# Performance work log

Measured on AMD Instinct MI355X. Metric: run time of the kernel, lower is better.

Reference implementation:

```python
import jax, jax.numpy as jnp
import numpy as np
from jax import lax

B = 2
H = W = 128          # resolution
N = H * W            # 16384 tokens
C = 128              # in_channels
C2 = C // 2          # 64, attention dim
G = 16               # window_size
HEADS = 8
HDIM = C2 // HEADS   # 8
EPS = 1e-5
DN = ('NCHW', 'OIHW', 'NCHW')


def setup_inputs():
    key = jax.random.key(0)
    ks = jax.random.split(key, 16)
    r = lambda i, shape, s=0.02: jax.random.normal(ks[i], shape, jnp.float32) * s
    z = lambda shape: jnp.zeros(shape, jnp.float32)
    o = lambda shape: jnp.ones(shape, jnp.float32)
    return {
        'x_C': jax.random.normal(ks[0], (B, N, C), jnp.float32),
        'x_T': jax.random.normal(ks[1], (B, N, C), jnp.float32),
        # S_conv = depthwise 3x3 + pointwise 1x1
        'conv1_dw': r(2, (C, 1, 3, 3)), 'conv1_dw_b': z((C,)),
        'conv1_pw': r(3, (C, C, 1, 1)), 'conv1_pw_b': z((C,)),
        'bn1_gamma': o((C,)), 'bn1_beta': z((C,)),
        'bn1_mean': r(4, (C,), 0.1), 'bn1_var': jnp.abs(r(5, (C,), 0.1)) + 1.0,
        'enc_W': r(6, (C, C2)), 'enc_b': z((C2,)),
        'pos': r(7, (1, N, C2)),
        'ln_gamma': o((C2,)), 'ln_beta': z((C2,)),
        'qkv_W': r(8, (C2, 3 * C2)),                      # qkv_bias=False
        'proj_W': r(9, (C2, C2)), 'proj_b': z((C2,)),
        'ffn_W1': r(10, (C2, C2)), 'ffn_b1': z((C2,)),
        'ffn_W2': r(11, (C2, C2)), 'ffn_b2': z((C2,)),
        'dec_W': r(12, (C2, C)), 'dec_b': z((C,)),
    }


def _ln(x, g, b):
    m = jnp.mean(x, -1, keepdims=True)
    v = jnp.var(x, -1, keepdims=True)
    return (x - m) * jax.lax.rsqrt(v + EPS) * g + b


def _win_part(x):  # (B,N,C2) -> (B*nW, G*G, C2)
    x = x.reshape(B, H // G, G, W // G, G, C2).transpose(0, 1, 3, 2, 4, 5)
    return x.reshape(-1, G * G, C2)


def _win_rev(x):  # (B*nW, G*G, C2) -> (B,N,C2)
    x = x.reshape(B, H // G, W // G, G, G, C2).transpose(0, 1, 3, 2, 4, 5)
    return x.reshape(B, N, C2)


def reference(x_C, x_T, conv1_dw, conv1_dw_b, conv1_pw, conv1_pw_b,
              bn1_gamma, bn1_beta, bn1_mean, bn1_var,
              enc_W, enc_b, pos, ln_gamma, ln_beta, qkv_W,
              proj_W, proj_b, ffn_W1, ffn_b1, ffn_W2, ffn_b2, dec_W, dec_b):
    cb = lambda a: a[None, :, None, None]
    # ---- CNN branch on x_C: S_conv -> BN(eval) -> ReLU, residual
    xC = x_C.reshape(B, H, W, C).transpose(0, 3, 1, 2)  # NCHW
    h = lax.conv_general_dilated(xC, conv1_dw, (1, 1), 'SAME',
                                 feature_group_count=C, dimension_numbers=DN) + cb(conv1_dw_b)
    h = lax.conv_general_dilated(h, conv1_pw, (1, 1), 'SAME',
                                 dimension_numbers=DN) + cb(conv1_pw_b)
    h = (h - cb(bn1_mean)) * cb(bn1_gamma * jax.lax.rsqrt(bn1_var + EPS)) + cb(bn1_beta)
    x1 = jax.nn.relu(h) + xC
    # ---- x_T branch: source overwrites conv/bn outputs -> x2 = relu(x_T) + x_T
    xT = x_T.reshape(B, H, W, C).transpose(0, 3, 1, 2)
    x2 = jax.nn.relu(xT) + xT
    # ---- flatten to tokens, encode + positional embedding
    x = x1.transpose(0, 2, 3, 1).reshape(B, N, C)
    y = x2.transpose(0, 2, 3, 1).reshape(B, N, C)
    x_poi = x @ enc_W + enc_b + pos
    y_poi = y @ enc_W + enc_b + pos
    # ---- window partition + LayerNorm
    wx = _ln(_win_part(x_poi), ln_gamma, ln_beta)
    wy = _ln(_win_part(y_poi), ln_gamma, ln_beta)
    # ---- dual-stream windowed attention (cross values)
    scale = HDIM ** -0.5
    def qkv(t):
        q, k, v = jnp.split(t @ qkv_W, 3, axis=-1)
        re = lambda a: a.reshape(-1, G * G, HEADS, HDIM).transpose(0, 2, 1, 3)
        return re(q), re(k), re(v)
    q, k, v = qkv(wx)
    q1, k1, v1 = qkv(wy)
    attn = jax.nn.softmax(jnp.einsum('bhid,bhjd->bhij', q * scale, k), axis=-1)
    attn1 = jax.nn.softmax(jnp.einsum('bhid,bhjd->bhij', q1 * scale, k1), axis=-1)
    ox = jnp.einsum('bhij,bhjd->bhid', attn, v1).transpose(0, 2, 1, 3).reshape(-1, G * G, C2)
    oy = jnp.einsum('bhij,bhjd->bhid', attn1, v).transpose(0, 2, 1, 3).reshape(-1, G * G, C2)
    ox = ox @ proj_W + proj_b + wx
    oy = oy @ proj_W + proj_b + wy
    # ---- window reverse + FFN (pre-LN, residual)
    x = _win_rev(ox)
    y = _win_rev(oy)
    ffn = lambda t: jax.nn.relu(_ln(t, ln_gamma, ln_beta) @ ffn_W1 + ffn_b1) @ ffn_W2 + ffn_b2
    x = x + ffn(x)
    y = y + ffn(y)
    # ---- decode back to C channels; to_3d(reshape) is identity on (B,N,C)
    return (x @ dec_W + dec_b) + (y @ dec_W + dec_b)
```

## Files before the change

### kernel.cpp

```cpp
#include <hip/hip_runtime.h>
#include <hip/hip_bf16.h>
#include <math.h>

#define EPSF 1e-5f
#define KSCL 0.51010090329771713f

#if __has_builtin(__builtin_amdgcn_exp2f)
#define EXP2(x) __builtin_amdgcn_exp2f(x)
#else
#define EXP2(x) exp2f(x)
#endif

typedef __attribute__((ext_vector_type(8))) short short8;
typedef __attribute__((ext_vector_type(16))) float f32x16;

__device__ __forceinline__ unsigned int f2bf(float f) {
    union { float f; unsigned int i; } u; u.f = f;
    unsigned int r = u.i + 0x7FFFu + ((u.i >> 16) & 1u);
    return r >> 16;
}
__device__ __forceinline__ unsigned cvtpk(float a, float b) {
    unsigned r;
    asm("v_cvt_pk_bf16_f32 %0, %1, %2" : "=v"(r) : "v"(a), "v"(b));
    return r;
}
__device__ __forceinline__ void bbuild(const unsigned pk[8], int lh,
                                       short8& B0, short8& B1) {
    unsigned xs[8];
    #pragma unroll
    for (int i = 0; i < 8; ++i) xs[i] = (unsigned)__shfl_xor((int)pk[i], 32);
    uint4 w0, w1;
    w0.x = lh ? xs[2] : pk[0]; w0.y = lh ? xs[3] : pk[1];
    w0.z = lh ? pk[2] : xs[0]; w0.w = lh ? pk[3] : xs[1];
    w1.x = lh ? xs[6] : pk[4]; w1.y = lh ? xs[7] : pk[5];
    w1.z = lh ? pk[6] : xs[4]; w1.w = lh ? pk[7] : xs[5];
    B0 = __builtin_bit_cast(short8, w0);
    B1 = __builtin_bit_cast(short8, w1);
}

__global__ __launch_bounds__(256) void k_dwconv(
    const float* __restrict__ xC, const float* __restrict__ dwW,
    const float* __restrict__ dwB, unsigned short* __restrict__ xdwb,
    const float* __restrict__ qkvW, const float* __restrict__ pw,
    const float* __restrict__ pwb, const float* __restrict__ gam,
    const float* __restrict__ bet, const float* __restrict__ mean,
    const float* __restrict__ var, const float* __restrict__ projW,
    const float* __restrict__ W1, const float* __restrict__ W2,
    const float* __restrict__ decW,
    unsigned short* __restrict__ qkvWT, unsigned short* __restrict__ weff,
    float* __restrict__ beff, unsigned short* __restrict__ projWTn,
    unsigned short* __restrict__ W1Tn, unsigned short* __restrict__ W2Tn,
    unsigned short* __restrict__ decTn)
{
    int tid = threadIdx.x;
    int bid = blockIdx.x;
    if (bid >= 1024) {
        int pid = (bid - 1024) * 256 + tid;
        if (pid < 12288) {
            int o = pid >> 6, c = pid & 63;
            qkvWT[pid] = (unsigned short)f2bf(qkvW[c * 192 + o]);
        } else if (pid < 28672) {
            int i = pid - 12288;
            int co = i >> 7;
            float sc = gam[co] * rsqrtf(var[co] + EPSF);
            weff[i] = (unsigned short)f2bf(pw[i] * sc);
        } else if (pid < 32768) {
            int i = pid - 28672, m = i >> 6, c = i & 63;
            projWTn[i] = (unsigned short)f2bf(projW[c * 64 + m]);
        } else if (pid < 36864) {
            int i = pid - 32768, m = i >> 6, c = i & 63;
            W1Tn[i] = (unsigned short)f2bf(W1[c * 64 + m]);
        } else if (pid < 40960) {
            int i = pid - 36864, m = i >> 6, c = i & 63;
            W2Tn[i] = (unsigned short)f2bf(W2[c * 64 + m]);
        } else if (pid < 49152) {
            int i = pid - 40960, m = i >> 6, c = i & 63;
            decTn[i] = (unsigned short)f2bf(decW[c * 128 + m]);
        } else if (pid < 49280) {
            int i = pid - 49152;
            float sc = gam[i] * rsqrtf(var[i] + EPSF);
            beff[i] = (pwb[i] - mean[i]) * sc + bet[i];
        }
        return;
    }
    __shared__ float s_w[128 * 9];
    __shared__ float s_bias[128];
    for (int i = tid; i < 128 * 9; i += 256) s_w[i] = dwW[i];
    if (tid < 128) s_bias[tid] = dwB[tid];
    __syncthreads();
    int idx = bid * 256 + tid;
    int c4 = (idx & 31) * 4;
    int pg = idx >> 5;
    int t0 = pg * 4;
    int b = t0 >> 14, n = t0 & 16383;
    int row = n >> 7, col0 = n & 127;
    float vb[3][6][4];
    #pragma unroll
    for (int ky = 0; ky < 3; ++ky) {
        int r = row + ky - 1;
        #pragma unroll
        for (int cx = 0; cx < 6; ++cx) {
            int cl = col0 + cx - 1;
            if ((unsigned)r < 128u && (unsigned)cl < 128u) {
                *(float4*)&vb[ky][cx][0] =
                    *(const float4*)&xC[((size_t)(b << 14) + (r << 7) + cl) * 128 + c4];
            } else {
                vb[ky][cx][0] = 0.f; vb[ky][cx][1] = 0.f; vb[ky][cx][2] = 0.f; vb[ky][cx][3] = 0.f;
            }
        }
    }
    float acc[4][4];
    #pragma unroll
    for (int p = 0; p < 4; ++p)
        #pragma unroll
        for (int j = 0; j < 4; ++j) acc[p][j] = s_bias[c4 + j];
    #pragma unroll
    for (int ky = 0; ky < 3; ++ky)
        #pragma unroll
        for (int kx = 0; kx < 3; ++kx)
            #pragma unroll
            for (int j = 0; j < 4; ++j) {
                float w = s_w[(c4 + j) * 9 + ky * 3 + kx];
                #pragma unroll
                for (int p = 0; p < 4; ++p)
                    acc[p][j] = fmaf(w, vb[ky][p + kx][j], acc[p][j]);
            }
    #pragma unroll
    for (int p = 0; p < 4; ++p) {
        uint2 o;
        o.x = f2bf(acc[p][0]) | (f2bf(acc[p][1]) << 16);
        o.y = f2bf(acc[p][2]) | (f2bf(acc[p][3]) << 16);
        *(uint2*)&xdwb[((size_t)t0 + p) * 128 + c4] = o;
    }
}

__global__ __launch_bounds__(256) void k_pw(
    const unsigned short* __restrict__ xdwb, const float* __restrict__ xC,
    const unsigned short* __restrict__ weff, const float* __restrict__ beff,
    float* __restrict__ x1)
{
    int tid = threadIdx.x;
    int wv = tid >> 6, lane = tid & 63, l31 = lane & 31, lh = lane >> 5;
    int wr = wv >> 1, wc = wv & 1;
    int T0 = blockIdx.x * 64;
    int ta = T0 + wr * 32 + l31;
    short8 af[8];
    #pragma unroll
    for (int ks = 0; ks < 8; ++ks)
        af[ks] = *(const short8*)&xdwb[(size_t)ta * 128 + ks * 16 + lh * 8];
    #pragma unroll
    for (int nt = 0; nt < 2; ++nt) {
        int co = wc * 64 + nt * 32 + l31;
        f32x16 acc = {};
        #pragma unroll
        for (int ks = 0; ks < 8; ++ks) {
            short8 bfr = *(const short8*)&weff[(size_t)co * 128 + ks * 16 + lh * 8];
            acc = __builtin_amdgcn_mfma_f32_32x32x16_bf16(af[ks], bfr, acc, 0, 0, 0);
        }
        float be = beff[co];
        #pragma unroll
        for (int r = 0; r < 16; ++r) {
            int tt = T0 + wr * 32 + (r & 3) + 8 * (r >> 2) + 4 * lh;
            float v = fmaxf(acc[r] + be, 0.f) + xC[(size_t)tt * 128 + co];
            x1[(size_t)tt * 128 + co] = v;
        }
    }
}

__global__ __launch_bounds__(512) void k_encln(
    const float* __restrict__ x1, const float* __restrict__ xT,
    const float* __restrict__ encW, const float* __restrict__ encb,
    const float* __restrict__ pos, const float* __restrict__ lng,
    const float* __restrict__ lnb, float* __restrict__ wx, float* __restrict__ wy,
    unsigned short* __restrict__ wxb, unsigned short* __restrict__ wyb)
{
    __shared__ float s_in[64 * 128];
    __shared__ float s_w[128 * 64];
    int tid = threadIdx.x;
    int T0 = blockIdx.x * 64;
    int stream = blockIdx.y;
    for (int i = tid; i < 2048; i += 512) ((float4*)s_w)[i] = ((const float4*)encW)[i];
    if (stream == 0) {
        for (int i = tid; i < 2048; i += 512)
            ((float4*)s_in)[i] = ((const float4*)(x1 + (size_t)T0 * 128))[i];
    } else {
        for (int i = tid; i < 2048; i += 512) {
            float4 v = ((const float4*)(xT + (size_t)T0 * 128))[i];
            float4 o;
            o.x = v.x > 0.f ? 2.f * v.x : v.x;
            o.y = v.y > 0.f ? 2.f * v.y : v.y;
            o.z = v.z > 0.f ? 2.f * v.z : v.z;
            o.w = v.w > 0.f ? 2.f * v.w : v.w;
            ((float4*)s_in)[i] = o;
        }
    }
    __syncthreads();
    int q = tid & 15, o4 = q * 4;
    int tg = tid >> 4;
    float acc[2][4] = {};
    for (int ci = 0; ci < 128; ++ci) {
        float4 w = *(const float4*)&s_w[ci * 64 + o4];
        #pragma unroll
        for (int i = 0; i < 2; ++i) {
            float xin = s_in[(tg * 2 + i) * 128 + ci];
            acc[i][0] = fmaf(xin, w.x, acc[i][0]);
            acc[i][1] = fmaf(xin, w.y, acc[i][1]);
            acc[i][2] = fmaf(xin, w.z, acc[i][2]);
            acc[i][3] = fmaf(xin, w.w, acc[i][3]);
        }
    }
    float4 eb = *(const float4*)&encb[o4];
    float4 g  = *(const float4*)&lng[o4];
    float4 bb = *(const float4*)&lnb[o4];
    float* dst = stream == 0 ? wx : wy;
    unsigned short* dstb = stream == 0 ? wxb : wyb;
    #pragma unroll
    for (int i = 0; i < 2; ++i) {
        int t = T0 + tg * 2 + i;
        int n = t & 16383;
        float4 pv = *(const float4*)&pos[(size_t)n * 64 + o4];
        float v0 = acc[i][0] + eb.x + pv.x;
        float v1 = acc[i][1] + eb.y + pv.y;
        float v2 = acc[i][2] + eb.z + pv.z;
        float v3 = acc[i][3] + eb.w + pv.w;
        float sm = v0 + v1 + v2 + v3;
        float sq = v0 * v0 + v1 * v1 + v2 * v2 + v3 * v3;
        #pragma unroll
        for (int off = 1; off < 16; off <<= 1) {
            sm += __shfl_xor(sm, off);
            sq += __shfl_xor(sq, off);
        }
        float m = sm * (1.f / 64.f);
        float vr = sq * (1.f / 64.f) - m * m;
        float rs = rsqrtf(fmaxf(vr, 0.f) + EPSF);
        float4 o;
        o.x = (v0 - m) * rs * g.x + bb.x;
        o.y = (v1 - m) * rs * g.y + bb.y;
        o.z = (v2 - m) * rs * g.z + bb.z;
        o.w = (v3 - m) * rs * g.w + bb.w;
        *(float4*)&dst[(size_t)t * 64 + o4] = o;
        uint2 ob;
        ob.x = f2bf(o.x) | (f2bf(o.y) << 16);
        ob.y = f2bf(o.z) | (f2bf(o.w) << 16);
        *(uint2*)&dstb[(size_t)t * 64 + o4] = ob;
    }
}

__global__ __launch_bounds__(256) void k_qkv(
    const unsigned short* __restrict__ wxb, const unsigned short* __restrict__ wyb,
    const unsigned short* __restrict__ qkvWT,
    unsigned short* __restrict__ qk, unsigned short* __restrict__ vT)
{
    int tid = threadIdx.x;
    int wv = tid >> 6, lane = tid & 63, l31 = lane & 31, lh = lane >> 5;
    int s = blockIdx.y;
    int T0 = blockIdx.x * 128;
    int b = T0 >> 14;
    int row = (T0 & 16383) >> 7;
    const unsigned short* src = s ? wyb : wxb;
    int t = T0 + wv * 32 + l31;
    short8 bfr[4];
    #pragma unroll
    for (int ks = 0; ks < 4; ++ks)
        bfr[ks] = *(const short8*)&src[(size_t)t * 64 + ks * 16 + lh * 8];
    int cp = wv * 32 + l31;
    int wid = ((row >> 4) << 3) + (cp >> 4);
    int p = ((row & 15) << 4) + (cp & 15);
    size_t cb = (size_t)(s * 2 + b) * 512 + wid;
    #pragma unroll
    for (int nt = 0; nt < 6; ++nt) {
        f32x16 acc = {};
        #pragma unroll
        for (int ks = 0; ks < 4; ++ks) {
            short8 afr = *(const short8*)&qkvWT[(size_t)(nt * 32 + l31) * 64 + ks * 16 + lh * 8];
            acc = __builtin_amdgcn_mfma_f32_32x32x16_bf16(afr, bfr[ks], acc, 0, 0, 0);
        }
        if (nt < 4) {
            const float scl = nt < 2 ? 1.f : KSCL;
            const int sec = nt < 2 ? 0 : 1;
            #pragma unroll
            for (int g = 0; g < 4; ++g) {
                int head = (nt & 1) * 4 + g;
                unsigned short* rec = qk + (cb + head * 64) * 4096;
                float f0 = acc[4 * g + 0] * scl, f1 = acc[4 * g + 1] * scl;
                float f2 = acc[4 * g + 2] * scl, f3 = acc[4 * g + 3] * scl;
                unsigned u01 = cvtpk(f0, f1), u23 = cvtpk(f2, f3);
                int off = p * 16 + sec * 8 + 4 * lh;
                *(unsigned*)(rec + off) = u01;
                *(unsigned*)(rec + off + 2) = u23;
            }
        } else {
            #pragma unroll
            for (int g = 0; g < 4; ++g) {
                int head = (nt - 4) * 4 + g;
                unsigned short* vrec = vT + (cb + head * 64) * 2048;
                int d0 = 4 * lh;
                vrec[(d0 + 0) * 256 + p] = (unsigned short)f2bf(acc[4 * g + 0]);
                vrec[(d0 + 1) * 256 + p] = (unsigned short)f2bf(acc[4 * g + 1]);
                vrec[(d0 + 2) * 256 + p] = (unsigned short)f2bf(acc[4 * g + 2]);
                vrec[(d0 + 3) * 256 + p] = (unsigned short)f2bf(acc[4 * g + 3]);
            }
        }
    }
}

__global__ __launch_bounds__(256) void k_attn(
    const unsigned short* __restrict__ qk, const unsigned short* __restrict__ vT,
    float* __restrict__ ox, float* __restrict__ oy)
{
    int tid = threadIdx.x;
    int wave = tid >> 6, lane = tid & 63;
    int lh = lane >> 5, l31 = lane & 31;
    int bx = blockIdx.x;
    int s = bx >> 10;
    int r = bx & 1023;
    int head = (r >> 6) & 7, wid = r & 63, b = r >> 9;
    const unsigned short* qbase = qk + ((size_t)s * 1024 + r) * 4096;
    const unsigned short* vbase = vT + ((size_t)(s ^ 1) * 1024 + r) * 2048;

    short8 qf[2];
    #pragma unroll
    for (int qt = 0; qt < 2; ++qt) {
        uint4 v = {0u, 0u, 0u, 0u};
        if (lh == 0) v = *(const uint4*)(qbase + (size_t)(wave * 64 + qt * 32 + l31) * 16);
        qf[qt] = __builtin_bit_cast(short8, v);
    }
    f32x16 acc[2];
    #pragma unroll
    for (int qt = 0; qt < 2; ++qt) acc[qt] = (f32x16){};
    const unsigned ONES = 0x3F803F80u;

    for (int jt = 0; jt < 8; ++jt) {
        uint4 kv = {0u, 0u, 0u, 0u};
        if (lh == 0) kv = *(const uint4*)(qbase + (size_t)(jt * 32 + l31) * 16 + 8);
        short8 kf = __builtin_bit_cast(short8, kv);
        uint2 a0 = {ONES, ONES}, a1 = {ONES, ONES}, a2 = {ONES, ONES}, a3 = {ONES, ONES};
        if (l31 < 8) {
            const unsigned short* vp = vbase + l31 * 256 + jt * 32 + lh * 4;
            a0 = *(const uint2*)vp;
            a1 = *(const uint2*)(vp + 8);
            a2 = *(const uint2*)(vp + 16);
            a3 = *(const uint2*)(vp + 24);
        }
        uint4 vaw = {a0.x, a0.y, a1.x, a1.y};
        uint4 vbw = {a2.x, a2.y, a3.x, a3.y};
        short8 vf0 = __builtin_bit_cast(short8, vaw);
        short8 vf1 = __builtin_bit_cast(short8, vbw);
        #pragma unroll
        for (int qt = 0; qt < 2; ++qt) {
            f32x16 c = __builtin_amdgcn_mfma_f32_32x32x16_bf16(kf, qf[qt], (f32x16){}, 0, 0, 0);
            float p[16];
            #pragma unroll
            for (int i = 0; i < 16; ++i) p[i] = EXP2(c[i]);
            unsigned pk[8];
            #pragma unroll
            for (int i = 0; i < 8; ++i) pk[i] = cvtpk(p[2 * i], p[2 * i + 1]);
            uint4 bw0 = {pk[0], pk[1], pk[2], pk[3]};
            uint4 bw1 = {pk[4], pk[5], pk[6], pk[7]};
            short8 B0 = __builtin_bit_cast(short8, bw0);
            short8 B1 = __builtin_bit_cast(short8, bw1);
            acc[qt] = __builtin_amdgcn_mfma_f32_32x32x16_bf16(vf0, B0, acc[qt], 0, 0, 0);
            acc[qt] = __builtin_amdgcn_mfma_f32_32x32x16_bf16(vf1, B1, acc[qt], 0, 0, 0);
        }
    }
    float* dst = s ? oy : ox;
    #pragma unroll
    for (int qt = 0; qt < 2; ++qt) {
        float inv = 1.f / acc[qt][4];
        int p = wave * 64 + qt * 32 + l31;
        int orow = (wid >> 3) * 16 + (p >> 4);
        int ocol = (wid & 7) * 16 + (p & 15);
        size_t t = (size_t)b * 16384 + orow * 128 + ocol;
        float4 o;
        o.x = acc[qt][0] * inv; o.y = acc[qt][1] * inv;
        o.z = acc[qt][2] * inv; o.w = acc[qt][3] * inv;
        *(float4*)&dst[t * 64 + head * 8 + lh * 4] = o;
    }
}

__global__ __launch_bounds__(256) void k_fusedec(
    const float* __restrict__ ox, const float* __restrict__ oy,
    const float* __restrict__ wx, const float* __restrict__ wy,
    const unsigned short* __restrict__ projWTn, const float* __restrict__ projb,
    const unsigned short* __restrict__ W1Tn, const float* __restrict__ b1,
    const unsigned short* __restrict__ W2Tn, const float* __restrict__ b2,
    const unsigned short* __restrict__ decTn, const float* __restrict__ decb,
    const float* __restrict__ lng, const float* __restrict__ lnb,
    float* __restrict__ out)
{
    int tid = threadIdx.x;
    int wv = tid >> 6, l31 = tid & 31, lh = (tid >> 5) & 1;
    int t = blockIdx.x * 128 + wv * 32 + l31;
    f32x16 zacc[2];
    zacc[0] = (f32x16){}; zacc[1] = (f32x16){};
    #pragma unroll 1
    for (int s = 0; s < 2; ++s) {
        const float* osrc = s ? oy : ox;
        const float* wsrc = s ? wy : wx;
        short8 bo[4];
        #pragma unroll
        for (int kap = 0; kap < 4; ++kap) {
            float4 f0 = *(const float4*)&osrc[(size_t)t * 64 + kap * 16 + lh * 8];
            float4 f1 = *(const float4*)&osrc[(size_t)t * 64 + kap * 16 + lh * 8 + 4];
            uint4 w;
            w.x = cvtpk(f0.x, f0.y); w.y = cvtpk(f0.z, f0.w);
            w.z = cvtpk(f1.x, f1.y); w.w = cvtpk(f1.z, f1.w);
            bo[kap] = __builtin_bit_cast(short8, w);
        }
        f32x16 a1[2];
        #pragma unroll
        for (int ta = 0; ta < 2; ++ta) {
            f32x16 acc = {};
            #pragma unroll
            for (int kap = 0; kap < 4; ++kap) {
                short8 af = *(const short8*)&projWTn[(size_t)(ta * 32 + l31) * 64 + kap * 16 + lh * 8];
                acc = __builtin_amdgcn_mfma_f32_32x32x16_bf16(af, bo[kap], acc, 0, 0, 0);
            }
            #pragma unroll
            for (int g = 0; g < 4; ++g) {
                int c0 = ta * 32 + g * 8 + lh * 4;
                float4 pb = *(const float4*)&projb[c0];
                float4 wr = *(const float4*)&wsrc[(size_t)t * 64 + c0];
                acc[g * 4 + 0] += pb.x + wr.x;
                acc[g * 4 + 1] += pb.y + wr.y;
                acc[g * 4 + 2] += pb.z + wr.z;
                acc[g * 4 + 3] += pb.w + wr.w;
            }
            a1[ta] = acc;
        }
        float sm = 0.f, sq = 0.f;
        #pragma unroll
        for (int ta = 0; ta < 2; ++ta)
            #pragma unroll
            for (int r = 0; r < 16; ++r) { float v = a1[ta][r]; sm += v; sq += v * v; }
        sm += __shfl_xor(sm, 32); sq += __shfl_xor(sq, 32);
        float mu = sm * (1.f / 64.f);
        float rs = rsqrtf(fmaxf(sq * (1.f / 64.f) - mu * mu, 0.f) + EPSF);
        unsigned pku[2][8];
        #pragma unroll
        for (int ta = 0; ta < 2; ++ta)
            #pragma unroll
            for (int g = 0; g < 4; ++g) {
                int c0 = ta * 32 + g * 8 + lh * 4;
                float4 gg = *(const float4*)&lng[c0];
                float4 bb = *(const float4*)&lnb[c0];
                float u0 = (a1[ta][g * 4 + 0] - mu) * rs * gg.x + bb.x;
                float u1 = (a1[ta][g * 4 + 1] - mu) * rs * gg.y + bb.y;
                float u2 = (a1[ta][g * 4 + 2] - mu) * rs * gg.z + bb.z;
                float u3 = (a1[ta][g * 4 + 3] - mu) * rs * gg.w + bb.w;
                pku[ta][g * 2]     = cvtpk(u0, u1);
                pku[ta][g * 2 + 1] = cvtpk(u2, u3);
            }
        short8 Bu[4];
        bbuild(pku[0], lh, Bu[0], Bu[1]);
        bbuild(pku[1], lh, Bu[2], Bu[3]);
        unsigned pkh[2][8];
        #pragma unroll
        for (int th = 0; th < 2; ++th) {
            f32x16 acc = {};
            #pragma unroll
            for (int kap = 0; kap < 4; ++kap) {
                short8 af = *(const short8*)&W1Tn[(size_t)(th * 32 + l31) * 64 + kap * 16 + lh * 8];
                acc = __builtin_amdgcn_mfma_f32_32x32x16_bf16(af, Bu[kap], acc, 0, 0, 0);
            }
            #pragma unroll
            for (int g = 0; g < 4; ++g) {
                int c0 = th * 32 + g * 8 + lh * 4;
                float4 bb = *(const float4*)&b1[c0];
                float h0 = fmaxf(acc[g * 4 + 0] + bb.x, 0.f);
                float h1 = fmaxf(acc[g * 4 + 1] + bb.y, 0.f);
                float h2 = fmaxf(acc[g * 4 + 2] + bb.z, 0.f);
                float h3 = fmaxf(acc[g * 4 + 3] + bb.w, 0.f);
                pkh[th][g * 2]     = cvtpk(h0, h1);
                pkh[th][g * 2 + 1] = cvtpk(h2, h3);
            }
        }
        short8 Bh[4];
        bbuild(pkh[0], lh, Bh[0], Bh[1]);
        bbuild(pkh[1], lh, Bh[2], Bh[3]);
        #pragma unroll
        for (int ta = 0; ta < 2; ++ta) {
            f32x16 a3 = a1[ta];
            #pragma unroll
            for (int g = 0; g < 4; ++g) {
                int c0 = ta * 32 + g * 8 + lh * 4;
                float4 bb = *(const float4*)&b2[c0];
                a3[g * 4 + 0] += bb.x; a3[g * 4 + 1] += bb.y;
                a3[g * 4 + 2] += bb.z; a3[g * 4 + 3] += bb.w;
            }
            #pragma unroll
            for (int kap = 0; kap < 4; ++kap) {
                short8 af = *(const short8*)&W2Tn[(size_t)(ta * 32 + l31) * 64 + kap * 16 + lh * 8];
                a3 = __builtin_amdgcn_mfma_f32_32x32x16_bf16(af, Bh[kap], a3, 0, 0, 0);
            }
            zacc[ta] += a3;
        }
    }
    unsigned pkz[2][8];
    #pragma unroll
    for (int ta = 0; ta < 2; ++ta)
        #pragma unroll
        for (int g = 0; g < 4; ++g) {
            pkz[ta][g * 2]     = cvtpk(zacc[ta][g * 4 + 0], zacc[ta][g * 4 + 1]);
            pkz[ta][g * 2 + 1] = cvtpk(zacc[ta][g * 4 + 2], zacc[ta][g * 4 + 3]);
        }
    short8 Bz[4];
    bbuild(pkz[0], lh, Bz[0], Bz[1]);
    bbuild(pkz[1], lh, Bz[2], Bz[3]);
    #pragma unroll
    for (int mu4 = 0; mu4 < 4; ++mu4) {
        f32x16 a4 = {};
        #pragma unroll
        for (int g = 0; g < 4; ++g) {
            int c0 = mu4 * 32 + g * 8 + lh * 4;
            float4 db = *(const float4*)&decb[c0];
            a4[g * 4 + 0] = 2.f * db.x; a4[g * 4 + 1] = 2.f * db.y;
            a4[g * 4 + 2] = 2.f * db.z; a4[g * 4 + 3] = 2.f * db.w;
        }
        #pragma unroll
        for (int kap = 0; kap < 4; ++kap) {
            short8 af = *(const short8*)&decTn[(size_t)(mu4 * 32 + l31) * 64 + kap * 16 + lh * 8];
            a4 = __builtin_amdgcn_mfma_f32_32x32x16_bf16(af, Bz[kap], a4, 0, 0, 0);
        }
        #pragma unroll
        for (int g = 0; g < 4; ++g) {
            int c0 = mu4 * 32 + g * 8 + lh * 4;
            float4 o;
            o.x = a4[g * 4 + 0]; o.y = a4[g * 4 + 1];
            o.z = a4[g * 4 + 2]; o.w = a4[g * 4 + 3];
            *(float4*)&out[(size_t)t * 128 + c0] = o;
        }
    }
}

extern "C" void kernel_launch(void* const* d_in, const int* in_sizes, int n_in,
                              void* d_out, int out_size, void* d_ws, size_t ws_size,
                              hipStream_t stream) {
    const float* x_C   = (const float*)d_in[0];
    const float* x_T   = (const float*)d_in[1];
    const float* dwW   = (const float*)d_in[2];
    const float* dwB   = (const float*)d_in[3];
    const float* pw    = (const float*)d_in[4];
    const float* pwb   = (const float*)d_in[5];
    const float* gam   = (const float*)d_in[6];
    const float* bet   = (const float*)d_in[7];
    const float* mean  = (const float*)d_in[8];
    const float* var   = (const float*)d_in[9];
    const float* encW  = (const float*)d_in[10];
    const float* encb  = (const float*)d_in[11];
    const float* pos   = (const float*)d_in[12];
    const float* lng   = (const float*)d_in[13];
    const float* lnb   = (const float*)d_in[14];
    const float* qkvW  = (const float*)d_in[15];
    const float* projW = (const float*)d_in[16];
    const float* projb = (const float*)d_in[17];
    const float* W1    = (const float*)d_in[18];
    const float* b1    = (const float*)d_in[19];
    const float* W2    = (const float*)d_in[20];
    const float* b2    = (const float*)d_in[21];
    const float* decW  = (const float*)d_in[22];
    const float* decb  = (const float*)d_in[23];
    float* out = (float*)d_out;

    float* ws = (float*)d_ws;
    unsigned short* xdwb = (unsigned short*)ws;
    float* x1   = ws + 2097152;
    unsigned short* qkb  = (unsigned short*)(ws + 6291456);
    unsigned short* vTb  = (unsigned short*)(ws + 10485760);
    float* wx   = ws + 12582912;
    float* wy   = ws + 14680064;
    unsigned short* wxb = (unsigned short*)(ws + 16777216);
    unsigned short* wyb = (unsigned short*)(ws + 17825792);
    float* ox   = ws + 18874368;
    float* oy   = ws + 20971520;
    unsigned short* qkvWT   = (unsigned short*)(ws + 23068672);
    unsigned short* weff    = (unsigned short*)(ws + 23074816);
    float*          beff    = ws + 23083008;
    unsigned short* projWTn = (unsigned short*)(ws + 23083136);
    unsigned short* W1Tn    = (unsigned short*)(ws + 23085184);
    unsigned short* W2Tn    = (unsigned short*)(ws + 23087232);
    unsigned short* decTn   = (unsigned short*)(ws + 23089280);

    k_dwconv<<<1217, 256, 0, stream>>>(x_C, dwW, dwB, xdwb, qkvW, pw, pwb,
                                       gam, bet, mean, var, projW, W1, W2, decW,
                                       qkvWT, weff, beff, projWTn, W1Tn, W2Tn, decTn);
    k_pw<<<512, 256, 0, stream>>>(xdwb, x_C, weff, beff, x1);
    k_encln<<<dim3(512, 2), 512, 0, stream>>>(x1, x_T, encW, encb, pos, lng, lnb,
                                              wx, wy, wxb, wyb);
    k_qkv<<<dim3(256, 2), 256, 0, stream>>>(wxb, wyb, qkvWT, qkb, vTb);
    k_attn<<<2048, 256, 0, stream>>>(qkb, vTb, ox, oy);
    k_fusedec<<<256, 256, 0, stream>>>(ox, oy, wx, wy, projWTn, projb,
                                       W1Tn, b1, W2Tn, b2, decTn, decb,
                                       lng, lnb, out);
}
```

Before: 113.6 us.

## Move encoder projection to bf16 MFMA and drop fp32 intermediates

The encoder linear plus LayerNorm kernel, previously a scalar FP32 shared-memory GEMM, now runs on bf16 MFMA 32x32x16 with the encoder weight pre-transposed to bf16 in the prep kernel. The pointwise-conv output x1 is now stored as bf16 instead of fp32. The fp32 copies of wx/wy are no longer written, and the fused decode kernel reads the residual from the bf16 buffers. This cuts memory traffic and ALU time in the encoder stage, at the cost of extra bf16 rounding on x1 and on the attention residual.

Result: faster. 100.8 us (-11.3%).

```diff
diff --git a/kernel.cpp b/kernel.cpp
--- a/kernel.cpp
+++ b/kernel.cpp
@@ -14,6 +14,9 @@
 typedef __attribute__((ext_vector_type(8))) short short8;
 typedef __attribute__((ext_vector_type(16))) float f32x16;
 
+__device__ __forceinline__ float bf2f(unsigned short u) {
+    union { unsigned int i; float f; } x; x.i = ((unsigned int)u) << 16; return x.f;
+}
 __device__ __forceinline__ unsigned int f2bf(float f) {
     union { float f; unsigned int i; } u; u.f = f;
     unsigned int r = u.i + 0x7FFFu + ((u.i >> 16) & 1u);
@@ -46,11 +49,11 @@
     const float* __restrict__ bet, const float* __restrict__ mean,
     const float* __restrict__ var, const float* __restrict__ projW,
     const float* __restrict__ W1, const float* __restrict__ W2,
-    const float* __restrict__ decW,
+    const float* __restrict__ decW, const float* __restrict__ encW,
     unsigned short* __restrict__ qkvWT, unsigned short* __restrict__ weff,
     float* __restrict__ beff, unsigned short* __restrict__ projWTn,
     unsigned short* __restrict__ W1Tn, unsigned short* __restrict__ W2Tn,
-    unsigned short* __restrict__ decTn)
+    unsigned short* __restrict__ decTn, unsigned short* __restrict__ encWTn)
 {
     int tid = threadIdx.x;
     int bid = blockIdx.x;
@@ -76,8 +79,11 @@
         } else if (pid < 49152) {
             int i = pid - 40960, m = i >> 6, c = i & 63;
             decTn[i] = (unsigned short)f2bf(decW[c * 128 + m]);
-        } else if (pid < 49280) {
-            int i = pid - 49152;
+        } else if (pid < 57344) {
+            int i = pid - 49152, m = i >> 7, c = i & 127;
+            encWTn[i] = (unsigned short)f2bf(encW[c * 64 + m]);
+        } else if (pid < 57472) {
+            int i = pid - 57344;
             float sc = gam[i] * rsqrtf(var[i] + EPSF);
             beff[i] = (pwb[i] - mean[i]) * sc + bet[i];
         }
@@ -137,7 +143,7 @@
 __global__ __launch_bounds__(256) void k_pw(
     const unsigned short* __restrict__ xdwb, const float* __restrict__ xC,
     const unsigned short* __restrict__ weff, const float* __restrict__ beff,
-    float* __restrict__ x1)
+    unsigned short* __restrict__ x1b)
 {
     int tid = threadIdx.x;
     int wv = tid >> 6, lane = tid & 63, l31 = lane & 31, lh = lane >> 5;
@@ -162,88 +168,91 @@
         for (int r = 0; r < 16; ++r) {
             int tt = T0 + wr * 32 + (r & 3) + 8 * (r >> 2) + 4 * lh;
             float v = fmaxf(acc[r] + be, 0.f) + xC[(size_t)tt * 128 + co];
-            x1[(size_t)tt * 128 + co] = v;
-        }
-    }
-}
-
-__global__ __launch_bounds__(512) void k_encln(
-    const float* __restrict__ x1, const float* __restrict__ xT,
-    const float* __restrict__ encW, const float* __restrict__ encb,
+            x1b[(size_t)tt * 128 + co] = (unsigned short)f2bf(v);
+        }
+    }
+}
+
+__global__ __launch_bounds__(256) void k_enc(
+    const unsigned short* __restrict__ x1b, const float* __restrict__ xT,
+    const unsigned short* __restrict__ encWTn, const float* __restrict__ encb,
     const float* __restrict__ pos, const float* __restrict__ lng,
-    const float* __restrict__ lnb, float* __restrict__ wx, float* __restrict__ wy,
+    const float* __restrict__ lnb,
     unsigned short* __restrict__ wxb, unsigned short* __restrict__ wyb)
 {
-    __shared__ float s_in[64 * 128];
-    __shared__ float s_w[128 * 64];
     int tid = threadIdx.x;
-    int T0 = blockIdx.x * 64;
-    int stream = blockIdx.y;
-    for (int i = tid; i < 2048; i += 512) ((float4*)s_w)[i] = ((const float4*)encW)[i];
-    if (stream == 0) {
-        for (int i = tid; i < 2048; i += 512)
-            ((float4*)s_in)[i] = ((const float4*)(x1 + (size_t)T0 * 128))[i];
+    int wv = tid >> 6, l31 = tid & 31, lh = (tid >> 5) & 1;
+    int s = blockIdx.y;
+    int t = blockIdx.x * 128 + wv * 32 + l31;
+    int n = t & 16383;
+    short8 bf[8];
+    if (s == 0) {
+        #pragma unroll
+        for (int ks = 0; ks < 8; ++ks)
+            bf[ks] = *(const short8*)&x1b[(size_t)t * 128 + ks * 16 + lh * 8];
     } else {
-        for (int i = tid; i < 2048; i += 512) {
-            float4 v = ((const float4*)(xT + (size_t)T0 * 128))[i];
-            float4 o;
-            o.x = v.x > 0.f ? 2.f * v.x : v.x;
-            o.y = v.y > 0.f ? 2.f * v.y : v.y;
-            o.z = v.z > 0.f ? 2.f * v.z : v.z;
-            o.w = v.w > 0.f ? 2.f * v.w : v.w;
-            ((float4*)s_in)[i] = o;
-        }
-    }
-    __syncthreads();
-    int q = tid & 15, o4 = q * 4;
-    int tg = tid >> 4;
-    float acc[2][4] = {};
-    for (int ci = 0; ci < 128; ++ci) {
-        float4 w = *(const float4*)&s_w[ci * 64 + o4];
-        #pragma unroll
-        for (int i = 0; i < 2; ++i) {
-            float xin = s_in[(tg * 2 + i) * 128 + ci];
-            acc[i][0] = fmaf(xin, w.x, acc[i][0]);
-            acc[i][1] = fmaf(xin, w.y, acc[i][1]);
-            acc[i][2] = fmaf(xin, w.z, acc[i][2]);
-            acc[i][3] = fmaf(xin, w.w, acc[i][3]);
-        }
-    }
-    float4 eb = *(const float4*)&encb[o4];
-    float4 g  = *(const float4*)&lng[o4];
-    float4 bb = *(const float4*)&lnb[o4];
-    float* dst = stream == 0 ? wx : wy;
-    unsigned short* dstb = stream == 0 ? wxb : wyb;
-    #pragma unroll
-    for (int i = 0; i < 2; ++i) {
-        int t = T0 + tg * 2 + i;
-        int n = t & 16383;
-        float4 pv = *(const float4*)&pos[(size_t)n * 64 + o4];
-        float v0 = acc[i][0] + eb.x + pv.x;
-        float v1 = acc[i][1] + eb.y + pv.y;
-        float v2 = acc[i][2] + eb.z + pv.z;
-        float v3 = acc[i][3] + eb.w + pv.w;
-        float sm = v0 + v1 + v2 + v3;
-        float sq = v0 * v0 + v1 * v1 + v2 * v2 + v3 * v3;
-        #pragma unroll
-        for (int off = 1; off < 16; off <<= 1) {
-            sm += __shfl_xor(sm, off);
-            sq += __shfl_xor(sq, off);
-        }
-        float m = sm * (1.f / 64.f);
-        float vr = sq * (1.f / 64.f) - m * m;
-        float rs = rsqrtf(fmaxf(vr, 0.f) + EPSF);
-        float4 o;
-        o.x = (v0 - m) * rs * g.x + bb.x;
-        o.y = (v1 - m) * rs * g.y + bb.y;
-        o.z = (v2 - m) * rs * g.z + bb.z;
-        o.w = (v3 - m) * rs * g.w + bb.w;
-        *(float4*)&dst[(size_t)t * 64 + o4] = o;
-        uint2 ob;
-        ob.x = f2bf(o.x) | (f2bf(o.y) << 16);
-        ob.y = f2bf(o.z) | (f2bf(o.w) << 16);
-        *(uint2*)&dstb[(size_t)t * 64 + o4] = ob;
-    }
+        #pragma unroll
+        for (int ks = 0; ks < 8; ++ks) {
+            float4 f0 = *(const float4*)&xT[(size_t)t * 128 + ks * 16 + lh * 8];
+            float4 f1 = *(const float4*)&xT[(size_t)t * 128 + ks * 16 + lh * 8 + 4];
+            float r0 = f0.x > 0.f ? 2.f * f0.x : f0.x;
+            float r1 = f0.y > 0.f ? 2.f * f0.y : f0.y;
+            float r2 = f0.z > 0.f ? 2.f * f0.z : f0.z;
+            float r3 = f0.w > 0.f ? 2.f * f0.w : f0.w;
+            float r4 = f1.x > 0.f ? 2.f * f1.x : f1.x;
+            float r5 = f1.y > 0.f ? 2.f * f1.y : f1.y;
+            float r6 = f1.z > 0.f ? 2.f * f1.z : f1.z;
+            float r7 = f1.w > 0.f ? 2.f * f1.w : f1.w;
+            uint4 w;
+            w.x = cvtpk(r0, r1); w.y = cvtpk(r2, r3);
+            w.z = cvtpk(r4, r5); w.w = cvtpk(r6, r7);
+            bf[ks] = __builtin_bit_cast(short8, w);
+        }
+    }
+    f32x16 xm[2];
+    #pragma unroll
+    for (int ta = 0; ta < 2; ++ta) {
+        f32x16 acc = {};
+        #pragma unroll
+        for (int ks = 0; ks < 8; ++ks) {
+            short8 af = *(const short8*)&encWTn[(size_t)(ta * 32 + l31) * 128 + ks * 16 + lh * 8];
+            acc = __builtin_amdgcn_mfma_f32_32x32x16_bf16(af, bf[ks], acc, 0, 0, 0);
+        }
+        #pragma unroll
+        for (int g = 0; g < 4; ++g) {
+            int c0 = ta * 32 + g * 8 + lh * 4;
+            float4 eb = *(const float4*)&encb[c0];
+            float4 pv = *(const float4*)&pos[(size_t)n * 64 + c0];
+            acc[g * 4 + 0] += eb.x + pv.x;
+            acc[g * 4 + 1] += eb.y + pv.y;
+            acc[g * 4 + 2] += eb.z + pv.z;
+            acc[g * 4 + 3] += eb.w + pv.w;
+        }
+        xm[ta] = acc;
+    }
+    float sm = 0.f, sq = 0.f;
+    #pragma unroll
+    for (int ta = 0; ta < 2; ++ta)
+        #pragma unroll
+        for (int r = 0; r < 16; ++r) { float v = xm[ta][r]; sm += v; sq += v * v; }
+    sm += __shfl_xor(sm, 32); sq += __shfl_xor(sq, 32);
+    float mu = sm * (1.f / 64.f);
+    float rs = rsqrtf(fmaxf(sq * (1.f / 64.f) - mu * mu, 0.f) + EPSF);
+    unsigned short* dstb = s ? wyb : wxb;
+    #pragma unroll
+    for (int ta = 0; ta < 2; ++ta)
+        #pragma unroll
+        for (int g = 0; g < 4; ++g) {
+            int c0 = ta * 32 + g * 8 + lh * 4;
+            float4 gg = *(const float4*)&lng[c0];
+            float4 bb = *(const float4*)&lnb[c0];
+            float u0 = (xm[ta][g * 4 + 0] - mu) * rs * gg.x + bb.x;
+            float u1 = (xm[ta][g * 4 + 1] - mu) * rs * gg.y + bb.y;
+            float u2 = (xm[ta][g * 4 + 2] - mu) * rs * gg.z + bb.z;
+            float u3 = (xm[ta][g * 4 + 3] - mu) * rs * gg.w + bb.w;
+            uint2 o; o.x = cvtpk(u0, u1); o.y = cvtpk(u2, u3);
+            *(uint2*)&dstb[(size_t)t * 64 + c0] = o;
+        }
 }
 
 __global__ __launch_bounds__(256) void k_qkv(
@@ -380,7 +389,7 @@
 
 __global__ __launch_bounds__(256) void k_fusedec(
     const float* __restrict__ ox, const float* __restrict__ oy,
-    const float* __restrict__ wx, const float* __restrict__ wy,
+    const unsigned short* __restrict__ wxb, const unsigned short* __restrict__ wyb,
     const unsigned short* __restrict__ projWTn, const float* __restrict__ projb,
     const unsigned short* __restrict__ W1Tn, const float* __restrict__ b1,
     const unsigned short* __restrict__ W2Tn, const float* __restrict__ b2,
@@ -396,7 +405,7 @@
     #pragma unroll 1
     for (int s = 0; s < 2; ++s) {
         const float* osrc = s ? oy : ox;
-        const float* wsrc = s ? wy : wx;
+        const unsigned short* wsrc = s ? wyb : wxb;
         short8 bo[4];
         #pragma unroll
         for (int kap = 0; kap < 4; ++kap) {
@@ -420,11 +429,11 @@
             for (int g = 0; g < 4; ++g) {
                 int c0 = ta * 32 + g * 8 + lh * 4;
                 float4 pb = *(const float4*)&projb[c0];
-                float4 wr = *(const float4*)&wsrc[(size_t)t * 64 + c0];
-                acc[g * 4 + 0] += pb.x + wr.x;
-                acc[g * 4 + 1] += pb.y + wr.y;
-                acc[g * 4 + 2] += pb.z + wr.z;
-                acc[g * 4 + 3] += pb.w + wr.w;
+                uint2 wr2 = *(const uint2*)&wsrc[(size_t)t * 64 + c0];
+                acc[g * 4 + 0] += pb.x + bf2f((unsigned short)(wr2.x & 0xffffu));
+                acc[g * 4 + 1] += pb.y + bf2f((unsigned short)(wr2.x >> 16));
+                acc[g * 4 + 2] += pb.z + bf2f((unsigned short)(wr2.y & 0xffffu));
+                acc[g * 4 + 3] += pb.w + bf2f((unsigned short)(wr2.y >> 16));
             }
             a1[ta] = acc;
         }
@@ -564,32 +573,32 @@
 
     float* ws = (float*)d_ws;
     unsigned short* xdwb = (unsigned short*)ws;
-    float* x1   = ws + 2097152;
-    unsigned short* qkb  = (unsigned short*)(ws + 6291456);
-    unsigned short* vTb  = (unsigned short*)(ws + 10485760);
-    float* wx   = ws + 12582912;
-    float* wy   = ws + 14680064;
-    unsigned short* wxb = (unsigned short*)(ws + 16777216);
-    unsigned short* wyb = (unsigned short*)(ws + 17825792);
-    float* ox   = ws + 18874368;
-    float* oy   = ws + 20971520;
-    unsigned short* qkvWT   = (unsigned short*)(ws + 23068672);
-    unsigned short* weff    = (unsigned short*)(ws + 23074816);
-    float*          beff    = ws + 23083008;
-    unsigned short* projWTn = (unsigned short*)(ws + 23083136);
-    unsigned short* W1Tn    = (unsigned short*)(ws + 23085184);
-    unsigned short* W2Tn    = (unsigned short*)(ws + 23087232);
-    unsigned short* decTn   = (unsigned short*)(ws + 23089280);
-
-    k_dwconv<<<1217, 256, 0, stream>>>(x_C, dwW, dwB, xdwb, qkvW, pw, pwb,
+    unsigned short* x1b  = (unsigned short*)(ws + 2097152);
+    unsigned short* qkb  = (unsigned short*)(ws + 4194304);
+    unsigned short* vTb  = (unsigned short*)(ws + 8388608);
+    unsigned short* wxb  = (unsigned short*)(ws + 10485760);
+    unsigned short* wyb  = (unsigned short*)(ws + 11534336);
+    float* ox   = ws + 12582912;
+    float* oy   = ws + 14680064;
+    unsigned short* qkvWT   = (unsigned short*)(ws + 16777216);
+    unsigned short* weff    = (unsigned short*)(ws + 16783360);
+    float*          beff    = ws + 16791552;
+    unsigned short* projWTn = (unsigned short*)(ws + 16791680);
+    unsigned short* W1Tn    = (unsigned short*)(ws + 16793728);
+    unsigned short* W2Tn    = (unsigned short*)(ws + 16795776);
+    unsigned short* decTn   = (unsigned short*)(ws + 16797824);
+    unsigned short* encWTn  = (unsigned short*)(ws + 16801920);
+
+    k_dwconv<<<1249, 256, 0, stream>>>(x_C, dwW, dwB, xdwb, qkvW, pw, pwb,
                                        gam, bet, mean, var, projW, W1, W2, decW,
-                                       qkvWT, weff, beff, projWTn, W1Tn, W2Tn, decTn);
-    k_pw<<<512, 256, 0, stream>>>(xdwb, x_C, weff, beff, x1);
-    k_encln<<<dim3(512, 2), 512, 0, stream>>>(x1, x_T, encW, encb, pos, lng, lnb,
-                                              wx, wy, wxb, wyb);
+                                       encW, qkvWT, weff, beff, projWTn,
+                                       W1Tn, W2Tn, decTn, encWTn);
+    k_pw<<<512, 256, 0, stream>>>(xdwb, x_C, weff, beff, x1b);
+    k_enc<<<dim3(256, 2), 256, 0, stream>>>(x1b, x_T, encWTn, encb, pos,
+                                            lng, lnb, wxb, wyb);
     k_qkv<<<dim3(256, 2), 256, 0, stream>>>(wxb, wyb, qkvWT, qkb, vTb);
     k_attn<<<2048, 256, 0, stream>>>(qkb, vTb, ox, oy);
-    k_fusedec<<<256, 256, 0, stream>>>(ox, oy, wx, wy, projWTn, projb,
+    k_fusedec<<<256, 256, 0, stream>>>(ox, oy, wxb, wyb, projWTn, projb,
                                        W1Tn, b1, W2Tn, b2, decTn, decb,
                                        lng, lnb, out);
 }
```
